# Performance work log

Hardware: AMD Instinct MI355X
Metric: run time of the kernel (lower is better)

Reference implementation:

```python
import jax, jax.numpy as jnp
import numpy as np

B, S, D = 2, 2048, 1024
H, A = 16, 64  # num_heads, attention_dim


def setup_inputs() -> dict:
    key = jax.random.key(0)
    ks = jax.random.split(key, 9)
    sd = D ** -0.5
    so = (H * A) ** -0.5
    return {
        "x": jax.random.normal(ks[0], (B, S, D), dtype=jnp.float32),
        "Wq": jax.random.normal(ks[1], (D, H * A), dtype=jnp.float32) * sd,
        "bq": jnp.zeros((H * A,), dtype=jnp.float32),
        "Wk": jax.random.normal(ks[2], (D, H * A), dtype=jnp.float32) * sd,
        "bk": jnp.zeros((H * A,), dtype=jnp.float32),
        "Wv": jax.random.normal(ks[3], (D, H * A), dtype=jnp.float32) * sd,
        "bv": jnp.zeros((H * A,), dtype=jnp.float32),
        "Wo": jax.random.normal(ks[4], (H * A, D), dtype=jnp.float32) * so,
        "bo": jnp.zeros((D,), dtype=jnp.float32),
    }


def reference(x, Wq, bq, Wk, bk, Wv, bv, Wo, bo):
    b, s, _ = x.shape
    # project and split heads: [b, s, H, A]
    q = (x @ Wq + bq).reshape(b, s, H, A)
    k = (x @ Wk + bk).reshape(b, s, H, A)
    v = (x @ Wv + bv).reshape(b, s, H, A)
    # scores [b, H, s, s]
    scores = jnp.einsum("bqhd,bkhd->bhqk", q, k) / jnp.sqrt(jnp.float32(A))
    weights = jax.nn.softmax(scores, axis=-1)
    attended = jnp.einsum("bhqk,bkhd->bqhd", weights, v).reshape(b, s, H * A)
    return attended @ Wo + bo
```

## Files before the change

### kernel.cpp

```cpp
#include <hip/hip_runtime.h>
#include <hip/hip_bf16.h>

typedef __attribute__((ext_vector_type(8))) short bf16x8;
typedef __attribute__((ext_vector_type(4))) float f32x4;

#define LOG2E 1.44269504088896f

extern "C" __device__ float __ocml_native_exp2_f32(float);

__device__ __forceinline__ unsigned short f2bf(float f) {
    union { float f; unsigned int u; } v; v.f = f;
    unsigned int r = v.u + 0x7FFF + ((v.u >> 16) & 1);
    return (unsigned short)(r >> 16);
}

__device__ __forceinline__ unsigned int pk_bf16(float lo, float hi) {
    unsigned int r;
    asm("v_cvt_pk_bf16_f32 %0, %1, %2" : "=v"(r) : "v"(lo), "v"(hi));
    return r;
}

typedef __attribute__((address_space(3))) unsigned int lds_uint;
typedef __attribute__((address_space(1))) const unsigned int glob_uint;
__device__ __forceinline__ void gl2lds16(const void* g, void* l) {
    __builtin_amdgcn_global_load_lds((glob_uint*)g, (lds_uint*)l, 16, 0, 0);
}

#define SYNC(vm)                                                             \
    asm volatile("s_waitcnt vmcnt(" #vm ")\n\ts_waitcnt lgkmcnt(0)" ::: "memory"); \
    __builtin_amdgcn_s_barrier();                                            \
    asm volatile("" ::: "memory")

__global__ __launch_bounds__(256) void cvt_bf16(const float* __restrict__ in,
                                                unsigned int* __restrict__ out, int n4) {
    int i = blockIdx.x * 256 + threadIdx.x;
    if (i >= n4) return;
    float4 v = ((const float4*)in)[i];
    uint2 o;
    o.x = pk_bf16(v.x, v.y);
    o.y = pk_bf16(v.z, v.w);
    ((uint2*)out)[i] = o;
}

__global__ __launch_bounds__(256) void transpose4_bf16(
    const float* __restrict__ w0, const float* __restrict__ w1,
    const float* __restrict__ w2, const float* __restrict__ w3,
    unsigned short* __restrict__ o0, unsigned short* __restrict__ o1,
    unsigned short* __restrict__ o2, unsigned short* __restrict__ o3) {
    const int z = blockIdx.z;
    const float* in = (z == 0) ? w0 : (z == 1) ? w1 : (z == 2) ? w2 : w3;
    unsigned short* out = (z == 0) ? o0 : (z == 1) ? o1 : (z == 2) ? o2 : o3;
    __shared__ float t[32][33];
    int tx = threadIdx.x & 31, ty = threadIdx.x >> 5;
    int r0 = blockIdx.y * 32, c0 = blockIdx.x * 32;
    for (int i = 0; i < 32; i += 8)
        t[ty + i][tx] = in[(size_t)(r0 + ty + i) * 1024 + c0 + tx];
    __syncthreads();
    for (int i = 0; i < 32; i += 8)
        out[(size_t)(c0 + ty + i) * 1024 + r0 + tx] = f2bf(t[tx][ty + i]);
}

__device__ __forceinline__ void gemm_core(const short* __restrict__ A,
                                          const short* __restrict__ BT,
                                          int K, int bm0, int bn0,
                                          short* sm, f32x4 acc[4][4]) {
    const int tid = threadIdx.x;
    const int lane = tid & 63;
    const int w = tid >> 6;
    const int wr0 = (w >> 1) * 64;
    const int wc0 = (w & 1) * 64;
    const int l15 = lane & 15, quad = lane >> 4;
    const int sr = lane >> 2;
    const int slog = (lane & 3) ^ (sr & 3) ^ (sr >> 2);

#pragma unroll
    for (int i = 0; i < 4; i++)
#pragma unroll
        for (int j = 0; j < 4; j++) acc[i][j] = (f32x4)0.f;

    const short* sp[4];
    int sdo[4];
#pragma unroll
    for (int i = 0; i < 4; i++) {
        int c = w * 4 + i;
        sp[i] = (c < 8) ? A + (size_t)(bm0 + c * 16 + sr) * K + slog * 8
                        : BT + (size_t)(bn0 + (c - 8) * 16 + sr) * K + slog * 8;
        sdo[i] = c * 512;
    }
    auto stage = [&](int buf) {
        short* bb = sm + buf * 8192;
#pragma unroll
        for (int i = 0; i < 4; i++) {
            gl2lds16(sp[i], bb + sdo[i]);
            sp[i] += 32;
        }
    };
    const int ph = (quad ^ (l15 & 3) ^ (l15 >> 2)) * 8;
    auto loadf = [&](bf16x8* af, bf16x8* bfr, int buf) {
        const short* Ab = sm + buf * 8192;
        const short* Bb = Ab + 4096;
#pragma unroll
        for (int im = 0; im < 4; im++)
            af[im] = *(const bf16x8*)&Ab[(wr0 + im * 16 + l15) * 32 + ph];
#pragma unroll
        for (int in = 0; in < 4; in++)
            bfr[in] = *(const bf16x8*)&Bb[(wc0 + in * 16 + l15) * 32 + ph];
        __builtin_amdgcn_sched_barrier(0);
    };
    auto computef = [&](const bf16x8* af, const bf16x8* bfr) {
        __builtin_amdgcn_s_setprio(1);
#pragma unroll
        for (int im = 0; im < 4; im++)
#pragma unroll
            for (int in = 0; in < 4; in++)
                acc[im][in] = __builtin_amdgcn_mfma_f32_16x16x32_bf16(af[im], bfr[in], acc[im][in], 0, 0, 0);
        __builtin_amdgcn_s_setprio(0);
    };

    stage(0); stage(1);
    asm volatile("s_waitcnt vmcnt(4)" ::: "memory");
    __builtin_amdgcn_s_barrier();
    asm volatile("" ::: "memory");

    bf16x8 aA[4], bA[4], aB[4], bB[4];
    loadf(aA, bA, 0);

    const int nt = K >> 5;
    int bs = 2, rb = 1;
    for (int t = 0; t < nt - 2; t += 2) {
        stage(bs); bs = (bs == 2) ? 0 : bs + 1;
        SYNC(4);
        loadf(aB, bB, rb); rb = (rb == 2) ? 0 : rb + 1;
        computef(aA, bA);
        stage(bs); bs = (bs == 2) ? 0 : bs + 1;
        SYNC(4);
        loadf(aA, bA, rb); rb = (rb == 2) ? 0 : rb + 1;
        computef(aB, bB);
    }
    SYNC(0);
    loadf(aB, bB, rb);
    computef(aA, bA);
    computef(aB, bB);
}

__global__ __launch_bounds__(256, 3) void gemm_qkv(
    const short* __restrict__ xb,
    const short* __restrict__ wqT, const short* __restrict__ wkT, const short* __restrict__ wvT,
    const float* __restrict__ bq, const float* __restrict__ bk, const float* __restrict__ bv,
    unsigned short* __restrict__ qb, unsigned short* __restrict__ kb, unsigned short* __restrict__ vTb) {
    __shared__ short sm[24576];
    const int z = blockIdx.z;
    const short* Amat = (z == 2) ? wvT : xb;
    const short* Bmat = (z == 0) ? wqT : (z == 1) ? wkT : xb;
    const float* bias = (z == 0) ? bq : (z == 1) ? bk : bv;
    const float scl = (z == 0) ? 0.125f * LOG2E : 1.f;
    const int bm0 = (z == 2) ? blockIdx.y * 128 : blockIdx.x * 128;
    const int bn0 = (z == 2) ? blockIdx.x * 128 : blockIdx.y * 128;
    f32x4 acc[4][4];
    gemm_core(Amat, Bmat, 1024, bm0, bn0, sm, acc);
    const int lane = threadIdx.x & 63, w = threadIdx.x >> 6;
    const int wr0 = (w >> 1) * 64, wc0 = (w & 1) * 64, l15 = lane & 15, quad = lane >> 4;
    if (z == 2) {
        for (int im = 0; im < 4; im++)
            for (int in = 0; in < 4; in++)
                for (int r = 0; r < 4; r++) {
                    int rowa = bm0 + wr0 + im * 16 + quad * 4 + r;
                    int colg = bn0 + wc0 + in * 16 + l15;
                    unsigned short ov = f2bf(acc[im][in][r] + bias[rowa]);
                    int b = colg >> 11, s = colg & 2047;
                    vTb[(size_t)b * 2097152 + (size_t)rowa * 2048 + s] = ov;
                }
    } else {
        for (int im = 0; im < 4; im++)
            for (int in = 0; in < 4; in++)
                for (int r = 0; r < 4; r++) {
                    int rowg = bm0 + wr0 + im * 16 + quad * 4 + r;
                    int colg = bn0 + wc0 + in * 16 + l15;
                    unsigned short ov = f2bf((acc[im][in][r] + bias[colg]) * scl);
                    int b = rowg >> 11, s = rowg & 2047;
                    int h = colg >> 6, a = colg & 63;
                    int bh = b * 16 + h;
                    if (z == 0) qb[((size_t)bh * 2048 + s) * 64 + a] = ov;
                    else        kb[((size_t)bh * 2048 + s) * 64 + a] = ov;
                }
    }
}

__global__ __launch_bounds__(256, 3) void gemm_out(
    const short* __restrict__ att, const short* __restrict__ woT,
    const float* __restrict__ bo, float* __restrict__ out) {
    __shared__ short sm[24576];
    const int bm0 = blockIdx.x * 128, bn0 = blockIdx.y * 128;
    f32x4 acc[4][4];
    gemm_core(att, woT, 1024, bm0, bn0, sm, acc);
    const int lane = threadIdx.x & 63, w = threadIdx.x >> 6;
    const int wr0 = (w >> 1) * 64, wc0 = (w & 1) * 64, l15 = lane & 15, quad = lane >> 4;
    for (int im = 0; im < 4; im++)
        for (int in = 0; in < 4; in++)
            for (int r = 0; r < 4; r++) {
                int rowg = bm0 + wr0 + im * 16 + quad * 4 + r;
                int colg = bn0 + wc0 + in * 16 + l15;
                out[(size_t)rowg * 1024 + colg] = acc[im][in][r] + bo[colg];
            }
}

__global__ __launch_bounds__(256, 2) void flash_attn(
    const unsigned short* __restrict__ qb, const unsigned short* __restrict__ kb,
    const unsigned short* __restrict__ vTb, unsigned short* __restrict__ att) {
    __shared__ short Ks[4][4096];
    __shared__ short Vs[4][4096];
    const int tid = threadIdx.x, lane = tid & 63, w = tid >> 6;
    const int l15 = lane & 15, quad = lane >> 4;
    const int lid = ((blockIdx.x & 7) << 6) | (blockIdx.x >> 3);
    const int q0 = (lid & 15) * 128;
    const int bh = lid >> 4;
    const size_t qkbase = (size_t)bh * 2048 * 64;
    const size_t vbase = (size_t)bh * 64 * 2048;
    const int sr = lane >> 3;
    const int slog = (lane & 7) ^ sr;
    const int l7 = l15 & 7;

    const unsigned short* sgp;
    int sgstep, sgr;
    short* sgb;
    if (w < 2) {
        sgp = kb + qkbase + (size_t)(w * 32 + sr) * 64 + slog * 8;
        sgstep = 4096; sgr = 512;
        sgb = &Ks[0][0] + w * 2048;
    } else {
        sgp = vTb + vbase + (size_t)((w - 2) * 32 + sr) * 2048 + slog * 8;
        sgstep = 64; sgr = 16384;
        sgb = &Vs[0][0] + (w - 2) * 2048;
    }
    auto stage_tile = [&](int buf) {
        short* sd = sgb + buf * 4096;
        gl2lds16(sgp, sd);
        gl2lds16(sgp + sgr, sd + 512);
        gl2lds16(sgp + 2 * sgr, sd + 1024);
        gl2lds16(sgp + 3 * sgr, sd + 1536);
        sgp += sgstep;
    };

    const int wq0 = w * 32;
    const int c0 = (quad ^ l7) * 8, c1 = c0 ^ 32;
    const int fb = l15 * 64;

    const unsigned short* qrow = qb + qkbase + (size_t)(q0 + wq0 + l15) * 64 + quad * 8;
    bf16x8 aq00 = *(const bf16x8*)qrow;
    bf16x8 aq01 = *(const bf16x8*)(qrow + 32);
    bf16x8 aq10 = *(const bf16x8*)(qrow + 1024);
    bf16x8 aq11 = *(const bf16x8*)(qrow + 1024 + 32);

    stage_tile(0); stage_tile(1); stage_tile(2);
    asm volatile("s_waitcnt vmcnt(4)" ::: "memory");
    __builtin_amdgcn_s_barrier();
    asm volatile("" ::: "memory");

    f32x4 o0[4], o1[4];
#pragma unroll
    for (int dt = 0; dt < 4; dt++) { o0[dt] = (f32x4)0.f; o1[dt] = (f32x4)0.f; }
    f32x4 ls0 = (f32x4)0.f, ls1 = (f32x4)0.f;

    auto load_kf = [&](bf16x8* kf, int buf) {
        const short* Kb = &Ks[0][0] + buf * 4096;
#pragma unroll
        for (int t = 0; t < 4; t++) {
            kf[2 * t]     = *(const bf16x8*)(Kb + fb + c0 + t * 1024);
            kf[2 * t + 1] = *(const bf16x8*)(Kb + fb + c1 + t * 1024);
        }
    };
    bf16x8 vf[8];
    auto load_vf = [&](int buf) {
        const short* Vb = &Vs[0][0] + buf * 4096;
#pragma unroll
        for (int t = 0; t < 4; t++) {
            vf[2 * t]     = *(const bf16x8*)(Vb + fb + c0 + t * 1024);
            vf[2 * t + 1] = *(const bf16x8*)(Vb + fb + c1 + t * 1024);
        }
    };

    auto qk = [&](const bf16x8* kf, f32x4* sc0, f32x4* sc1) {
        __builtin_amdgcn_s_setprio(1);
#pragma unroll
        for (int t = 0; t < 4; t++) {
            sc0[t] = __builtin_amdgcn_mfma_f32_16x16x32_bf16(kf[2 * t], aq00, (f32x4)0.f, 0, 0, 0);
            sc1[t] = __builtin_amdgcn_mfma_f32_16x16x32_bf16(kf[2 * t], aq10, (f32x4)0.f, 0, 0, 0);
        }
#pragma unroll
        for (int t = 0; t < 4; t++) {
            sc0[t] = __builtin_amdgcn_mfma_f32_16x16x32_bf16(kf[2 * t + 1], aq01, sc0[t], 0, 0, 0);
            sc1[t] = __builtin_amdgcn_mfma_f32_16x16x32_bf16(kf[2 * t + 1], aq11, sc1[t], 0, 0, 0);
        }
        __builtin_amdgcn_s_setprio(0);
    };

    auto smax = [&](f32x4 (&sc)[4], f32x4& lsr, bf16x8* bp) {
#pragma unroll
        for (int t = 0; t < 4; t++) {
#pragma unroll
            for (int r = 0; r < 4; r++) sc[t][r] = __ocml_native_exp2_f32(sc[t][r]);
            lsr += sc[t];
        }
#pragma unroll
        for (int t2 = 0; t2 < 2; t2++) {
            unsigned pa = pk_bf16(sc[2 * t2][0], sc[2 * t2][1]);
            unsigned pb = pk_bf16(sc[2 * t2][2], sc[2 * t2][3]);
            unsigned pc = pk_bf16(sc[2 * t2 + 1][0], sc[2 * t2 + 1][1]);
            unsigned pd = pk_bf16(sc[2 * t2 + 1][2], sc[2 * t2 + 1][3]);
            asm("v_permlane32_swap_b32 %0, %1" : "+v"(pa), "+v"(pc));
            asm("v_permlane32_swap_b32 %0, %1" : "+v"(pb), "+v"(pd));
            asm("v_permlane16_swap_b32 %0, %1" : "+v"(pa), "+v"(pc));
            asm("v_permlane16_swap_b32 %0, %1" : "+v"(pb), "+v"(pd));
            union { unsigned u[4]; bf16x8 v; } cvt;
            cvt.u[0] = pa; cvt.u[1] = pb; cvt.u[2] = pc; cvt.u[3] = pd;
            bp[t2] = cvt.v;
        }
    };

    auto pv = [&](const bf16x8* bp) {
        __builtin_amdgcn_s_setprio(1);
#pragma unroll
        for (int t2 = 0; t2 < 2; t2++)
#pragma unroll
            for (int dt = 0; dt < 4; dt++) {
                o0[dt] = __builtin_amdgcn_mfma_f32_16x16x32_bf16(vf[2 * dt + t2], bp[t2], o0[dt], 0, 0, 0);
                o1[dt] = __builtin_amdgcn_mfma_f32_16x16x32_bf16(vf[2 * dt + t2], bp[2 + t2], o1[dt], 0, 0, 0);
            }
        __builtin_amdgcn_s_setprio(0);
    };

    bf16x8 kfA[8], kfB[8];
    bf16x8 bpA[4], bpB[4];

    load_kf(kfA, 0);
    asm volatile("s_waitcnt lgkmcnt(0)" ::: "memory");
    __builtin_amdgcn_sched_barrier(0);

    auto step = [&](int t, const bf16x8* kfC, bf16x8* kfN, bf16x8* bpC,
                    const bf16x8* bpP, bool dokf, bool dopv, bool dostage) {
        if (dokf) load_kf(kfN, (t + 1) & 3);
        __builtin_amdgcn_sched_barrier(0);
        f32x4 sc0[4], sc1[4];
        qk(kfC, sc0, sc1);
        smax(sc0, ls0, bpC);
        smax(sc1, ls1, bpC + 2);
        if (dopv) pv(bpP);
        load_vf(t & 3);
        if (dostage) stage_tile((t + 3) & 3);
    };

    step(0, kfA, kfB, bpA, bpB, true, false, true); SYNC(4);
    for (int t = 1; t < 29; t += 2) {
        step(t,     kfB, kfA, bpB, bpA, true, true, true); SYNC(4);
        step(t + 1, kfA, kfB, bpA, bpB, true, true, true); SYNC(4);
    }
    step(29, kfB, kfA, bpB, bpA, true, true, false); SYNC(0);
    step(30, kfA, kfB, bpA, bpB, true, true, false); SYNC(0);
    step(31, kfB, kfA, bpB, bpA, false, true, false);
    asm volatile("s_waitcnt lgkmcnt(0)" ::: "memory");
    pv(bpB);

    const int b = bh >> 4, h = bh & 15;
    float l0 = (ls0[0] + ls0[1]) + (ls0[2] + ls0[3]);
    l0 += __shfl_xor(l0, 16);
    l0 += __shfl_xor(l0, 32);
    float inv0 = 1.f / l0;
    float l1 = (ls1[0] + ls1[1]) + (ls1[2] + ls1[3]);
    l1 += __shfl_xor(l1, 16);
    l1 += __shfl_xor(l1, 32);
    float inv1 = 1.f / l1;
    int s = q0 + wq0 + l15;
#pragma unroll
    for (int dt = 0; dt < 4; dt++) {
        int col = h * 64 + dt * 16 + quad * 4;
        uint2 pk;
        pk.x = pk_bf16(o0[dt][0] * inv0, o0[dt][1] * inv0);
        pk.y = pk_bf16(o0[dt][2] * inv0, o0[dt][3] * inv0);
        *(uint2*)&att[((size_t)b * 2048 + s) * 1024 + col] = pk;
        pk.x = pk_bf16(o1[dt][0] * inv1, o1[dt][1] * inv1);
        pk.y = pk_bf16(o1[dt][2] * inv1, o1[dt][3] * inv1);
        *(uint2*)&att[((size_t)b * 2048 + s + 16) * 1024 + col] = pk;
    }
}

extern "C" void kernel_launch(void* const* d_in, const int* in_sizes, int n_in,
                              void* d_out, int out_size, void* d_ws, size_t ws_size,
                              hipStream_t stream) {
    const float* x  = (const float*)d_in[0];
    const float* Wq = (const float*)d_in[1];
    const float* bq = (const float*)d_in[2];
    const float* Wk = (const float*)d_in[3];
    const float* bk = (const float*)d_in[4];
    const float* Wv = (const float*)d_in[5];
    const float* bv = (const float*)d_in[6];
    const float* Wo = (const float*)d_in[7];
    const float* bo = (const float*)d_in[8];
    float* out = (float*)d_out;

    short* ws  = (short*)d_ws;
    short* xb  = ws;
    short* wqT = ws + 4 * 1024 * 1024;
    short* wkT = wqT + 1024 * 1024;
    short* wvT = wkT + 1024 * 1024;
    short* woT = wvT + 1024 * 1024;
    short* qb  = woT + 1024 * 1024;
    short* kb  = qb + 4 * 1024 * 1024;
    short* vTb = kb + 4 * 1024 * 1024;
    short* att = vTb + 4 * 1024 * 1024;

    cvt_bf16<<<4096, 256, 0, stream>>>(x, (unsigned int*)xb, 1024 * 1024);
    transpose4_bf16<<<dim3(32, 32, 4), 256, 0, stream>>>(
        Wq, Wk, Wv, Wo,
        (unsigned short*)wqT, (unsigned short*)wkT,
        (unsigned short*)wvT, (unsigned short*)woT);
    gemm_qkv<<<dim3(32, 8, 3), 256, 0, stream>>>(xb, wqT, wkT, wvT, bq, bk, bv,
                                                 (unsigned short*)qb, (unsigned short*)kb,
                                                 (unsigned short*)vTb);
    flash_attn<<<512, 256, 0, stream>>>((const unsigned short*)qb,
                                        (const unsigned short*)kb,
                                        (const unsigned short*)vTb,
                                        (unsigned short*)att);
    gemm_out<<<dim3(32, 8), 256, 0, stream>>>(att, woT, bo, out);
}
```

Baseline: 178.0 us.

## Load V fragments directly from global, deepen K LDS ring to six buffers

The flash attention kernel stops staging V through LDS and has each lane load its V^T fragments straight from global memory into registers. The freed LDS holds a six-deep K ring buffer, and the step is reordered so the PV MFMA runs before QK. Barriers now occur once per two tiles, with vmcnt waits tuned per step. This aims to cut LDS traffic and barrier stalls, at the cost of more uncoalesced global loads and higher register pressure, with correctness resting on the hand-tuned wait counts.

```diff
diff --git a/kernel.cpp b/kernel.cpp
--- a/kernel.cpp
+++ b/kernel.cpp
@@ -26,8 +26,15 @@
     __builtin_amdgcn_global_load_lds((glob_uint*)g, (lds_uint*)l, 16, 0, 0);
 }
 
+#define VMW(n) asm volatile("s_waitcnt vmcnt(" #n ")" ::: "memory")
+
 #define SYNC(vm)                                                             \
     asm volatile("s_waitcnt vmcnt(" #vm ")\n\ts_waitcnt lgkmcnt(0)" ::: "memory"); \
+    __builtin_amdgcn_s_barrier();                                            \
+    asm volatile("" ::: "memory")
+
+#define SYNCB                                                                \
+    asm volatile("s_waitcnt lgkmcnt(0)" ::: "memory");                       \
     __builtin_amdgcn_s_barrier();                                            \
     asm volatile("" ::: "memory")
 
@@ -207,8 +214,7 @@
 __global__ __launch_bounds__(256, 2) void flash_attn(
     const unsigned short* __restrict__ qb, const unsigned short* __restrict__ kb,
     const unsigned short* __restrict__ vTb, unsigned short* __restrict__ att) {
-    __shared__ short Ks[4][4096];
-    __shared__ short Vs[4][4096];
+    __shared__ short Ks[6][4096];
     const int tid = threadIdx.x, lane = tid & 63, w = tid >> 6;
     const int l15 = lane & 15, quad = lane >> 4;
     const int lid = ((blockIdx.x & 7) << 6) | (blockIdx.x >> 3);
@@ -220,25 +226,13 @@
     const int slog = (lane & 7) ^ sr;
     const int l7 = l15 & 7;
 
-    const unsigned short* sgp;
-    int sgstep, sgr;
-    short* sgb;
-    if (w < 2) {
-        sgp = kb + qkbase + (size_t)(w * 32 + sr) * 64 + slog * 8;
-        sgstep = 4096; sgr = 512;
-        sgb = &Ks[0][0] + w * 2048;
-    } else {
-        sgp = vTb + vbase + (size_t)((w - 2) * 32 + sr) * 2048 + slog * 8;
-        sgstep = 64; sgr = 16384;
-        sgb = &Vs[0][0] + (w - 2) * 2048;
-    }
+    const unsigned short* sgp = kb + qkbase + (size_t)(w * 16 + sr) * 64 + slog * 8;
+    short* sgb = &Ks[0][0] + w * 1024;
     auto stage_tile = [&](int buf) {
         short* sd = sgb + buf * 4096;
         gl2lds16(sgp, sd);
-        gl2lds16(sgp + sgr, sd + 512);
-        gl2lds16(sgp + 2 * sgr, sd + 1024);
-        gl2lds16(sgp + 3 * sgr, sd + 1536);
-        sgp += sgstep;
+        gl2lds16(sgp + 512, sd + 512);
+        sgp += 4096;
     };
 
     const int wq0 = w * 32;
@@ -251,15 +245,17 @@
     bf16x8 aq10 = *(const bf16x8*)(qrow + 1024);
     bf16x8 aq11 = *(const bf16x8*)(qrow + 1024 + 32);
 
-    stage_tile(0); stage_tile(1); stage_tile(2);
-    asm volatile("s_waitcnt vmcnt(4)" ::: "memory");
-    __builtin_amdgcn_s_barrier();
-    asm volatile("" ::: "memory");
-
-    f32x4 o0[4], o1[4];
-#pragma unroll
-    for (int dt = 0; dt < 4; dt++) { o0[dt] = (f32x4)0.f; o1[dt] = (f32x4)0.f; }
-    f32x4 ls0 = (f32x4)0.f, ls1 = (f32x4)0.f;
+    const unsigned short* vp = vTb + vbase + (size_t)l15 * 2048 + quad * 8;
+    int kvo = 0;
+    bf16x8 vf[8];
+    auto load_vf = [&] {
+#pragma unroll
+        for (int dt = 0; dt < 4; dt++) {
+            vf[2 * dt]     = *(const bf16x8*)(vp + (size_t)dt * 32768 + kvo);
+            vf[2 * dt + 1] = *(const bf16x8*)(vp + (size_t)dt * 32768 + kvo + 32);
+        }
+        kvo += 64;
+    };
 
     auto load_kf = [&](bf16x8* kf, int buf) {
         const short* Kb = &Ks[0][0] + buf * 4096;
@@ -268,16 +264,13 @@
             kf[2 * t]     = *(const bf16x8*)(Kb + fb + c0 + t * 1024);
             kf[2 * t + 1] = *(const bf16x8*)(Kb + fb + c1 + t * 1024);
         }
-    };
-    bf16x8 vf[8];
-    auto load_vf = [&](int buf) {
-        const short* Vb = &Vs[0][0] + buf * 4096;
-#pragma unroll
-        for (int t = 0; t < 4; t++) {
-            vf[2 * t]     = *(const bf16x8*)(Vb + fb + c0 + t * 1024);
-            vf[2 * t + 1] = *(const bf16x8*)(Vb + fb + c1 + t * 1024);
-        }
-    };
+        __builtin_amdgcn_sched_barrier(0);
+    };
+
+    f32x4 o0[4], o1[4];
+#pragma unroll
+    for (int dt = 0; dt < 4; dt++) { o0[dt] = (f32x4)0.f; o1[dt] = (f32x4)0.f; }
+    f32x4 ls0 = (f32x4)0.f, ls1 = (f32x4)0.f;
 
     auto qk = [&](const bf16x8* kf, f32x4* sc0, f32x4* sc1) {
         __builtin_amdgcn_s_setprio(1);
@@ -332,32 +325,41 @@
     bf16x8 kfA[8], kfB[8];
     bf16x8 bpA[4], bpB[4];
 
-    load_kf(kfA, 0);
-    asm volatile("s_waitcnt lgkmcnt(0)" ::: "memory");
-    __builtin_amdgcn_sched_barrier(0);
-
-    auto step = [&](int t, const bf16x8* kfC, bf16x8* kfN, bf16x8* bpC,
-                    const bf16x8* bpP, bool dokf, bool dopv, bool dostage) {
-        if (dokf) load_kf(kfN, (t + 1) & 3);
-        __builtin_amdgcn_sched_barrier(0);
+    auto step = [&](bf16x8* kfC, bf16x8* kfN, bf16x8* bpC, const bf16x8* bpP,
+                    int nbuf, bool dokf, bool dopv, bool dostage, int sbuf) {
+        if (dokf) load_kf(kfN, nbuf);
+        if (dopv) pv(bpP);
+        load_vf();
         f32x4 sc0[4], sc1[4];
         qk(kfC, sc0, sc1);
-        smax(sc0, ls0, bpC);
-        smax(sc1, ls1, bpC + 2);
-        if (dopv) pv(bpP);
-        load_vf(t & 3);
-        if (dostage) stage_tile((t + 3) & 3);
-    };
-
-    step(0, kfA, kfB, bpA, bpB, true, false, true); SYNC(4);
-    for (int t = 1; t < 29; t += 2) {
-        step(t,     kfB, kfA, bpB, bpA, true, true, true); SYNC(4);
-        step(t + 1, kfA, kfB, bpA, bpB, true, true, true); SYNC(4);
+        smax(sc0, ls0, bpA == bpC ? bpA : bpB);
+        smax(sc1, ls1, (bpA == bpC ? bpA : bpB) + 2);
+        if (dostage) stage_tile(sbuf);
+    };
+
+    stage_tile(0); stage_tile(1); stage_tile(2); stage_tile(3);
+    VMW(4);
+    __builtin_amdgcn_s_barrier();
+    asm volatile("" ::: "memory");
+    load_kf(kfA, 0);
+
+    VMW(12); step(kfA, kfB, bpA, bpB, 1, true, false, true, 4);
+    VMW(12); step(kfB, kfA, bpB, bpA, 2, true, true,  true, 5);
+    SYNCB;
+    int nb = 3, sb = 0;
+    for (int it = 0; it < 13; it++) {
+        VMW(12); step(kfA, kfB, bpA, bpB, nb, true, true, true, sb);
+        nb = (nb == 5) ? 0 : nb + 1; sb = (sb == 5) ? 0 : sb + 1;
+        VMW(12); step(kfB, kfA, bpB, bpA, nb, true, true, true, sb);
+        nb = (nb == 5) ? 0 : nb + 1; sb = (sb == 5) ? 0 : sb + 1;
+        SYNCB;
     }
-    step(29, kfB, kfA, bpB, bpA, true, true, false); SYNC(0);
-    step(30, kfA, kfB, bpA, bpB, true, true, false); SYNC(0);
-    step(31, kfB, kfA, bpB, bpA, false, true, false);
-    asm volatile("s_waitcnt lgkmcnt(0)" ::: "memory");
+    VMW(12); step(kfA, kfB, bpA, bpB, nb, true, true, false, 0);
+    nb = (nb == 5) ? 0 : nb + 1;
+    VMW(10); step(kfB, kfA, bpB, bpA, nb, true, true, false, 0);
+    nb = (nb == 5) ? 0 : nb + 1;
+    VMW(8);  step(kfA, kfB, bpA, bpB, nb, true, true, false, 0);
+    step(kfB, kfA, bpB, bpA, 0, false, true, false, 0);
     pv(bpB);
 
     const int b = bh >> 4, h = bh & 15;
```

New measurement: 203.3 us. 1.14x slower.

## Enlarge GEMM tiles to 128x256 and simplify the LDS pipeline

Applied to the files above, without the earlier changes.

The QKV and output GEMMs move from 128x128 to 128x256 block tiles. Each wave now computes a 64x128 sub-tile, which raises MFMA work per LDS fragment load and halves the grid. The fragment double-buffering in registers is replaced by a single load-then-compute step per K tile, and occupancy drops to 2 blocks per CU because of the larger LDS and accumulator footprint. The risks are fewer blocks to fill the CUs (384 and 128 blocks) and less latency hiding, since fragment loads are no longer overlapped with MFMAs.

```diff
diff --git a/kernel.cpp b/kernel.cpp
--- a/kernel.cpp
+++ b/kernel.cpp
@@ -25,6 +25,8 @@
 __device__ __forceinline__ void gl2lds16(const void* g, void* l) {
     __builtin_amdgcn_global_load_lds((glob_uint*)g, (lds_uint*)l, 16, 0, 0);
 }
+
+#define VMW(n) asm volatile("s_waitcnt vmcnt(" #n ")" ::: "memory")
 
 #define SYNC(vm)                                                             \
     asm volatile("s_waitcnt vmcnt(" #vm ")\n\ts_waitcnt lgkmcnt(0)" ::: "memory"); \
@@ -63,12 +65,12 @@
 __device__ __forceinline__ void gemm_core(const short* __restrict__ A,
                                           const short* __restrict__ BT,
                                           int K, int bm0, int bn0,
-                                          short* sm, f32x4 acc[4][4]) {
+                                          short* sm, f32x4 acc[4][8]) {
     const int tid = threadIdx.x;
     const int lane = tid & 63;
     const int w = tid >> 6;
     const int wr0 = (w >> 1) * 64;
-    const int wc0 = (w & 1) * 64;
+    const int wc0 = (w & 1) * 128;
     const int l15 = lane & 15, quad = lane >> 4;
     const int sr = lane >> 2;
     const int slog = (lane & 3) ^ (sr & 3) ^ (sr >> 2);
@@ -76,93 +78,89 @@
 #pragma unroll
     for (int i = 0; i < 4; i++)
 #pragma unroll
-        for (int j = 0; j < 4; j++) acc[i][j] = (f32x4)0.f;
-
-    const short* sp[4];
-    int sdo[4];
-#pragma unroll
-    for (int i = 0; i < 4; i++) {
-        int c = w * 4 + i;
+        for (int j = 0; j < 8; j++) acc[i][j] = (f32x4)0.f;
+
+    const short* sp[6];
+    int sdo[6];
+#pragma unroll
+    for (int i = 0; i < 6; i++) {
+        int c = w * 6 + i;
         sp[i] = (c < 8) ? A + (size_t)(bm0 + c * 16 + sr) * K + slog * 8
                         : BT + (size_t)(bn0 + (c - 8) * 16 + sr) * K + slog * 8;
         sdo[i] = c * 512;
     }
     auto stage = [&](int buf) {
-        short* bb = sm + buf * 8192;
-#pragma unroll
-        for (int i = 0; i < 4; i++) {
+        short* bb = sm + buf * 12288;
+#pragma unroll
+        for (int i = 0; i < 6; i++) {
             gl2lds16(sp[i], bb + sdo[i]);
             sp[i] += 32;
         }
     };
     const int ph = (quad ^ (l15 & 3) ^ (l15 >> 2)) * 8;
-    auto loadf = [&](bf16x8* af, bf16x8* bfr, int buf) {
-        const short* Ab = sm + buf * 8192;
+    auto compute = [&](int buf) {
+        const short* Ab = sm + buf * 12288;
         const short* Bb = Ab + 4096;
+        bf16x8 af[4], bfr[8];
 #pragma unroll
         for (int im = 0; im < 4; im++)
             af[im] = *(const bf16x8*)&Ab[(wr0 + im * 16 + l15) * 32 + ph];
 #pragma unroll
-        for (int in = 0; in < 4; in++)
+        for (int in = 0; in < 8; in++)
             bfr[in] = *(const bf16x8*)&Bb[(wc0 + in * 16 + l15) * 32 + ph];
-        __builtin_amdgcn_sched_barrier(0);
-    };
-    auto computef = [&](const bf16x8* af, const bf16x8* bfr) {
         __builtin_amdgcn_s_setprio(1);
 #pragma unroll
         for (int im = 0; im < 4; im++)
 #pragma unroll
-            for (int in = 0; in < 4; in++)
+            for (int in = 0; in < 8; in++)
                 acc[im][in] = __builtin_amdgcn_mfma_f32_16x16x32_bf16(af[im], bfr[in], acc[im][in], 0, 0, 0);
         __builtin_amdgcn_s_setprio(0);
     };
 
     stage(0); stage(1);
-    asm volatile("s_waitcnt vmcnt(4)" ::: "memory");
+    VMW(6);
     __builtin_amdgcn_s_barrier();
     asm volatile("" ::: "memory");
 
-    bf16x8 aA[4], bA[4], aB[4], bB[4];
-    loadf(aA, bA, 0);
-
     const int nt = K >> 5;
-    int bs = 2, rb = 1;
-    for (int t = 0; t < nt - 2; t += 2) {
+    int bs = 2, bc = 0;
+    for (int t = 0; t < nt - 2; ++t) {
         stage(bs); bs = (bs == 2) ? 0 : bs + 1;
-        SYNC(4);
-        loadf(aB, bB, rb); rb = (rb == 2) ? 0 : rb + 1;
-        computef(aA, bA);
-        stage(bs); bs = (bs == 2) ? 0 : bs + 1;
-        SYNC(4);
-        loadf(aA, bA, rb); rb = (rb == 2) ? 0 : rb + 1;
-        computef(aB, bB);
-    }
+        compute(bc); bc = (bc == 2) ? 0 : bc + 1;
+        SYNC(6);
+    }
+    compute(bc); bc = (bc == 2) ? 0 : bc + 1;
     SYNC(0);
-    loadf(aB, bB, rb);
-    computef(aA, bA);
-    computef(aB, bB);
-}
-
-__global__ __launch_bounds__(256, 3) void gemm_qkv(
+    compute(bc);
+}
+
+__global__ __launch_bounds__(256, 2) void gemm_qkv(
     const short* __restrict__ xb,
     const short* __restrict__ wqT, const short* __restrict__ wkT, const short* __restrict__ wvT,
     const float* __restrict__ bq, const float* __restrict__ bk, const float* __restrict__ bv,
     unsigned short* __restrict__ qb, unsigned short* __restrict__ kb, unsigned short* __restrict__ vTb) {
-    __shared__ short sm[24576];
+    __shared__ short sm[36864];
     const int z = blockIdx.z;
     const short* Amat = (z == 2) ? wvT : xb;
     const short* Bmat = (z == 0) ? wqT : (z == 1) ? wkT : xb;
     const float* bias = (z == 0) ? bq : (z == 1) ? bk : bv;
     const float scl = (z == 0) ? 0.125f * LOG2E : 1.f;
-    const int bm0 = (z == 2) ? blockIdx.y * 128 : blockIdx.x * 128;
-    const int bn0 = (z == 2) ? blockIdx.x * 128 : blockIdx.y * 128;
-    f32x4 acc[4][4];
+    int bm0, bn0;
+    if (z == 2) {
+        int flat = blockIdx.y * 32 + blockIdx.x;
+        bm0 = (flat & 7) * 128;
+        bn0 = (flat >> 3) * 256;
+    } else {
+        bm0 = blockIdx.x * 128;
+        bn0 = blockIdx.y * 256;
+    }
+    f32x4 acc[4][8];
     gemm_core(Amat, Bmat, 1024, bm0, bn0, sm, acc);
     const int lane = threadIdx.x & 63, w = threadIdx.x >> 6;
-    const int wr0 = (w >> 1) * 64, wc0 = (w & 1) * 64, l15 = lane & 15, quad = lane >> 4;
+    const int wr0 = (w >> 1) * 64, wc0 = (w & 1) * 128, l15 = lane & 15, quad = lane >> 4;
     if (z == 2) {
         for (int im = 0; im < 4; im++)
-            for (int in = 0; in < 4; in++)
+            for (int in = 0; in < 8; in++)
                 for (int r = 0; r < 4; r++) {
                     int rowa = bm0 + wr0 + im * 16 + quad * 4 + r;
                     int colg = bn0 + wc0 + in * 16 + l15;
@@ -172,7 +170,7 @@
                 }
     } else {
         for (int im = 0; im < 4; im++)
-            for (int in = 0; in < 4; in++)
+            for (int in = 0; in < 8; in++)
                 for (int r = 0; r < 4; r++) {
                     int rowg = bm0 + wr0 + im * 16 + quad * 4 + r;
                     int colg = bn0 + wc0 + in * 16 + l15;
@@ -186,17 +184,17 @@
     }
 }
 
-__global__ __launch_bounds__(256, 3) void gemm_out(
+__global__ __launch_bounds__(256, 2) void gemm_out(
     const short* __restrict__ att, const short* __restrict__ woT,
     const float* __restrict__ bo, float* __restrict__ out) {
-    __shared__ short sm[24576];
-    const int bm0 = blockIdx.x * 128, bn0 = blockIdx.y * 128;
-    f32x4 acc[4][4];
+    __shared__ short sm[36864];
+    const int bm0 = blockIdx.x * 128, bn0 = blockIdx.y * 256;
+    f32x4 acc[4][8];
     gemm_core(att, woT, 1024, bm0, bn0, sm, acc);
     const int lane = threadIdx.x & 63, w = threadIdx.x >> 6;
-    const int wr0 = (w >> 1) * 64, wc0 = (w & 1) * 64, l15 = lane & 15, quad = lane >> 4;
+    const int wr0 = (w >> 1) * 64, wc0 = (w & 1) * 128, l15 = lane & 15, quad = lane >> 4;
     for (int im = 0; im < 4; im++)
-        for (int in = 0; in < 4; in++)
+        for (int in = 0; in < 8; in++)
             for (int r = 0; r < 4; r++) {
                 int rowg = bm0 + wr0 + im * 16 + quad * 4 + r;
                 int colg = bn0 + wc0 + in * 16 + l15;
@@ -252,7 +250,7 @@
     bf16x8 aq11 = *(const bf16x8*)(qrow + 1024 + 32);
 
     stage_tile(0); stage_tile(1); stage_tile(2);
-    asm volatile("s_waitcnt vmcnt(4)" ::: "memory");
+    VMW(4);
     __builtin_amdgcn_s_barrier();
     asm volatile("" ::: "memory");
 
@@ -413,12 +411,12 @@
         Wq, Wk, Wv, Wo,
         (unsigned short*)wqT, (unsigned short*)wkT,
         (unsigned short*)wvT, (unsigned short*)woT);
-    gemm_qkv<<<dim3(32, 8, 3), 256, 0, stream>>>(xb, wqT, wkT, wvT, bq, bk, bv,
+    gemm_qkv<<<dim3(32, 4, 3), 256, 0, stream>>>(xb, wqT, wkT, wvT, bq, bk, bv,
                                                  (unsigned short*)qb, (unsigned short*)kb,
                                                  (unsigned short*)vTb);
     flash_attn<<<512, 256, 0, stream>>>((const unsigned short*)qb,
                                         (const unsigned short*)kb,
                                         (const unsigned short*)vTb,
                                         (unsigned short*)att);
-    gemm_out<<<dim3(32, 8), 256, 0, stream>>>(att, woT, bo, out);
-}
+    gemm_out<<<dim3(32, 4), 256, 0, stream>>>(att, woT, bo, out);
+}
```

Result: slower. 190.9 us (+7.3%).
